# Kernel tuning notes

Measured on AMD Instinct MI355X. Metric: run time of the kernel, lower is better.

The kernel has to match this reference:

```python
import jax, jax.numpy as jnp
import numpy as np

EPS = 1e-5

def _layer_norm(x, gamma, beta):
    mu = jnp.mean(x, axis=-1, keepdims=True)
    var = jnp.mean(jnp.square(x - mu), axis=-1, keepdims=True)
    return (x - mu) * jax.lax.rsqrt(var + EPS) * gamma + beta

def setup_inputs() -> dict:
    key = jax.random.key(0)
    ks = jax.random.split(key, 6)
    B, D, H = 8192, 1024, 1024
    x = jax.random.normal(ks[0], (B, D), dtype=jnp.float32)
    h0 = jax.random.normal(ks[1], (B, H), dtype=jnp.float32)
    c0 = jax.random.normal(ks[2], (B, H), dtype=jnp.float32)
    # learned params (orthogonal init approximated by scaled normal for reference purposes)
    weight_h = jax.random.normal(ks[3], (H, 4 * H), dtype=jnp.float32) / np.sqrt(H)
    weight_x = jax.random.normal(ks[4], (D, 4 * H), dtype=jnp.float32) / np.sqrt(D)
    bias = jnp.zeros((4 * H,), dtype=jnp.float32).at[:H].set(1.0)  # forget-gate bias init to 1
    ln1_g = jnp.ones((4 * H,), jnp.float32); ln1_b = jnp.zeros((4 * H,), jnp.float32)
    ln2_g = jnp.ones((4 * H,), jnp.float32); ln2_b = jnp.zeros((4 * H,), jnp.float32)
    ln3_g = jnp.ones((H,), jnp.float32); ln3_b = jnp.zeros((H,), jnp.float32)
    return {"x": x, "h0": h0, "c0": c0, "weight_h": weight_h, "weight_x": weight_x,
            "bias": bias, "ln1_g": ln1_g, "ln1_b": ln1_b, "ln2_g": ln2_g, "ln2_b": ln2_b,
            "ln3_g": ln3_g, "ln3_b": ln3_b}

def reference(x, h0, c0, weight_h, weight_x, bias, ln1_g, ln1_b, ln2_g, ln2_b, ln3_g, ln3_b):
    # gates: [B, 4H] = LN(h0 @ Wh) + LN(x @ Wx) + bias
    gates = _layer_norm(h0 @ weight_h, ln1_g, ln1_b) + _layer_norm(x @ weight_x, ln2_g, ln2_b) + bias
    H = h0.shape[-1]
    f_g, i_g, o_g, c_g = jnp.split(gates, 4, axis=1)  # forget, in, out, cell
    c1 = jax.nn.sigmoid(f_g) * c0 + jax.nn.sigmoid(i_g) * jnp.tanh(c_g)
    h1 = jax.nn.sigmoid(o_g) * jnp.tanh(_layer_norm(c1, ln3_g, ln3_b))
    return (h1, c1)
```

## Files before the change

kernel.cpp:

```cpp
#include <hip/hip_runtime.h>
#include <cstdint>

#define B_ROWS 8192
#define KDIM 1024
#define N4 4096

typedef __attribute__((ext_vector_type(8))) short short8;
typedef __attribute__((ext_vector_type(4))) float float4v;

__device__ __forceinline__ unsigned short f2bf(float f) {
  union { float f; unsigned int u; } v; v.f = f;
  unsigned int r = v.u + 0x7fffu + ((v.u >> 16) & 1u);
  return (unsigned short)(r >> 16);
}

__device__ __forceinline__ float bf2f(unsigned short s) {
  union { unsigned int u; float f; } v; v.u = ((unsigned int)s) << 16;
  return v.f;
}

__device__ __forceinline__ void async16(const unsigned short* g, unsigned short* l) {
  auto gp = (const __attribute__((address_space(1))) unsigned int*)(uintptr_t)g;
  auto lp = (__attribute__((address_space(3))) unsigned int*)(unsigned int)(uintptr_t)l;
  __builtin_amdgcn_global_load_lds(gp, lp, 16, 0, 0);
}

__device__ __forceinline__ float sigm(float v) {
  return __builtin_amdgcn_rcpf(1.f + __builtin_amdgcn_exp2f(-1.44269504088896f * v));
}
__device__ __forceinline__ float tanh_f(float v) {
  return 1.f - 2.f * __builtin_amdgcn_rcpf(1.f + __builtin_amdgcn_exp2f(2.88539008177793f * v));
}


__global__ __launch_bounds__(256) void prep(
    const float* __restrict__ h0, const float* __restrict__ x,
    unsigned short* __restrict__ Ah, unsigned short* __restrict__ Ax,
    const float* __restrict__ Wh, const float* __restrict__ Wx,
    unsigned short* __restrict__ Wth, unsigned short* __restrict__ Wtx) {
  __shared__ float tile[32][33];
  const int bid = blockIdx.x;
  if (bid < 16384) {
    const float* in = (bid >= 8192) ? x : h0;
    unsigned short* out = (bid >= 8192) ? Ax : Ah;
    int i = ((bid & 8191) * 256 + threadIdx.x) * 4;
    float4 v = *(const float4*)(in + i);
    ushort4 o;
    o.x = f2bf(v.x); o.y = f2bf(v.y); o.z = f2bf(v.z); o.w = f2bf(v.w);
    *(ushort4*)(out + i) = o;
  } else {
    int b2 = bid - 16384;
    const float* W = (b2 >= 4096) ? Wx : Wh;
    unsigned short* Wt = (b2 >= 4096) ? Wtx : Wth;
    int r = b2 & 4095;
    int n0 = (r & 127) * 32;
    int k0 = (r >> 7) * 32;
    int tx = threadIdx.x & 31;
    int ty = threadIdx.x >> 5;
#pragma unroll
    for (int i = 0; i < 32; i += 8)
      tile[ty + i][tx] = W[(size_t)(k0 + ty + i) * N4 + n0 + tx];
    __syncthreads();
#pragma unroll
    for (int i = 0; i < 32; i += 8)
      Wt[(size_t)(n0 + ty + i) * KDIM + k0 + tx] = f2bf(tile[tx][ty + i]);
  }
}


#define LGKM0()  asm volatile("s_waitcnt lgkmcnt(0)" ::: "memory")
#define SCHED0() __builtin_amdgcn_sched_barrier(0)
#define BARRIER() __builtin_amdgcn_s_barrier()
#define VM4BAR() asm volatile("s_waitcnt vmcnt(4)\n\ts_barrier" ::: "memory")

__global__ __launch_bounds__(512, 2) void gemm_bf16(
    const unsigned short* __restrict__ Ah, const unsigned short* __restrict__ Wth,
    unsigned short* __restrict__ Uh,
    const unsigned short* __restrict__ Ax, const unsigned short* __restrict__ Wtx,
    unsigned short* __restrict__ Ux, int row0) {
  const unsigned short* A; const unsigned short* W; unsigned short* U;
  if (blockIdx.z == 0) { A = Ah; W = Wth; U = Uh; } else { A = Ax; W = Wtx; U = Ux; }

  __shared__ unsigned short ldsA[2 * 256 * 64];
  __shared__ unsigned short ldsB[2 * 256 * 64];

  const int tid = threadIdx.x;
  const int wave = tid >> 6;
  const int lane = tid & 63;
  const int wm2 = wave >> 2;
  const int wn4 = wave & 3;

  const int gx = N4 / 256;
  const int nwg = gx * (int)gridDim.y;
  const int f = (int)blockIdx.y * gx + (int)blockIdx.x;
  const int qq = nwg >> 3, rr = nwg & 7;
  const int xcd = f & 7, idx = f >> 3;
  const int wg = (xcd < rr) ? (xcd * (qq + 1) + idx)
                            : (rr * (qq + 1) + (xcd - rr) * qq + idx);
  const int bx = wg & (gx - 1);
  const int by = wg / gx;

  const int m0 = row0 + by * 256;
  const int n0 = bx * 256;

  const int r8 = lane >> 3;
  const int c8 = lane & 7;
  const int g8 = ((c8 - r8) & 7) * 8;
  const int aR = wave * 32;
  const int bR = wave * 32;

  const unsigned short* gA = A + (size_t)(m0 + aR + r8) * KDIM + g8;
  const unsigned short* gB = W + (size_t)(n0 + bR + r8) * KDIM + g8;

  const int lq = lane & 15, lh = lane >> 4;
  const int offA0 = (wm2 * 128 + lq) * 64 + ((lh + lq) & 7) * 8;
  const int offA1 = (wm2 * 128 + lq) * 64 + ((4 + lh + lq) & 7) * 8;
  const int offB0 = (wn4 * 64 + lq) * 64 + ((lh + lq) & 7) * 8;
  const int offB1 = (wn4 * 64 + lq) * 64 + ((4 + lh + lq) & 7) * 8;

  float4v acc[8][4];
  float4v zero = {0.f, 0.f, 0.f, 0.f};
#pragma unroll
  for (int i = 0; i < 8; ++i)
#pragma unroll
    for (int j = 0; j < 4; ++j) acc[i][j] = zero;

#define STAGE4(gp, lb, kk)                                        \
  do {                                                            \
    async16((gp) + (kk), (lb));                                   \
    async16((gp) + (kk) + 8 * KDIM, (lb) + 8 * 64);               \
    async16((gp) + (kk) + 16 * KDIM, (lb) + 16 * 64);             \
    async16((gp) + (kk) + 24 * KDIM, (lb) + 24 * 64);             \
  } while (0)

  STAGE4(gB, ldsB + bR * 64, 0);
  STAGE4(gA, ldsA + aR * 64, 0);
  STAGE4(gB, ldsB + 16384 + bR * 64, 64);
  VM4BAR();

  short8 aF0[8], aF1[8], bF0[4], bF1[4];

  for (int t = 0; t < KDIM / 64; ++t) {
    const unsigned short* sA = ldsA + (t & 1) * 16384;
    const unsigned short* sB = ldsB + (t & 1) * 16384;
    unsigned short* nA = (unsigned short*)ldsA + ((t + 1) & 1) * 16384;
    unsigned short* cB = (unsigned short*)ldsB + (t & 1) * 16384;
    const int kA = (t + 1) * 64;
    const int kB = (t + 2) * 64;

    STAGE4(gA, nA + aR * 64, kA);

#pragma unroll
    for (int mi = 0; mi < 8; ++mi) aF0[mi] = *(const short8*)(sA + offA0 + mi * 1024);
#pragma unroll
    for (int nj = 0; nj < 4; ++nj) bF0[nj] = *(const short8*)(sB + offB0 + nj * 1024);
#pragma unroll
    for (int mi = 0; mi < 8; ++mi) aF1[mi] = *(const short8*)(sA + offA1 + mi * 1024);
#pragma unroll
    for (int nj = 0; nj < 4; ++nj) bF1[nj] = *(const short8*)(sB + offB1 + nj * 1024);

    __builtin_amdgcn_s_setprio(1);
#pragma unroll
    for (int mi = 0; mi < 8; ++mi)
#pragma unroll
      for (int nj = 0; nj < 4; ++nj)
        acc[mi][nj] = __builtin_amdgcn_mfma_f32_16x16x32_bf16(aF0[mi], bF0[nj], acc[mi][nj], 0, 0, 0);
    __builtin_amdgcn_s_setprio(0);

    LGKM0(); SCHED0();
    BARRIER();

    STAGE4(gB, cB + bR * 64, kB);

    __builtin_amdgcn_s_setprio(1);
#pragma unroll
    for (int mi = 0; mi < 8; ++mi)
#pragma unroll
      for (int nj = 0; nj < 4; ++nj)
        acc[mi][nj] = __builtin_amdgcn_mfma_f32_16x16x32_bf16(aF1[mi], bF1[nj], acc[mi][nj], 0, 0, 0);
    __builtin_amdgcn_s_setprio(0);

    VM4BAR();
  }
  asm volatile("s_waitcnt vmcnt(0)" ::: "memory");

  const int colc = lane & 15;
  const int rowq = (lane >> 4) * 4;
  unsigned short* Ub = U + (size_t)(by * 256 + wm2 * 128 + rowq) * N4 + n0 + wn4 * 64 + colc;
#pragma unroll
  for (int mi = 0; mi < 8; ++mi)
#pragma unroll
    for (int r = 0; r < 4; ++r) {
      unsigned short* Urow = Ub + (size_t)(mi * 16 + r) * N4;
#pragma unroll
      for (int nj = 0; nj < 4; ++nj) Urow[nj * 16] = f2bf(acc[mi][nj][r]);
    }
}


__global__ __launch_bounds__(256) void fused_ln_lstm(
    const unsigned short* __restrict__ Uh, const unsigned short* __restrict__ Ux,
    const float* __restrict__ c0, const float* __restrict__ bias,
    const float* __restrict__ g1, const float* __restrict__ b1,
    const float* __restrict__ g2, const float* __restrict__ b2,
    const float* __restrict__ g3, const float* __restrict__ b3,
    float* __restrict__ h1o, float* __restrict__ c1o, int row0) {
  const int t = threadIdx.x;
  const int lane = t & 63;
  const int wv = t >> 6;
  const size_t rloc = blockIdx.x;
  const size_t rabs = rloc + (size_t)row0;

  const ushort4* uh = (const ushort4*)(Uh + rloc * N4);
  const ushort4* ux = (const ushort4*)(Ux + rloc * N4);
  float4 cold = ((const float4*)(c0 + rabs * KDIM))[t];

  float4 vh[4], vx[4];
  float sh = 0.f, qh = 0.f, sx = 0.f, qx = 0.f;
#pragma unroll
  for (int k = 0; k < 4; ++k) {
    ushort4 au = uh[k * 256 + t];
    float4 a; a.x = bf2f(au.x); a.y = bf2f(au.y); a.z = bf2f(au.z); a.w = bf2f(au.w);
    vh[k] = a;
    sh += (a.x + a.y) + (a.z + a.w);
    qh += a.x * a.x + a.y * a.y + a.z * a.z + a.w * a.w;
    ushort4 bu = ux[k * 256 + t];
    float4 b; b.x = bf2f(bu.x); b.y = bf2f(bu.y); b.z = bf2f(bu.z); b.w = bf2f(bu.w);
    vx[k] = b;
    sx += (b.x + b.y) + (b.z + b.w);
    qx += b.x * b.x + b.y * b.y + b.z * b.z + b.w * b.w;
  }
  __shared__ float red[4][4];
#pragma unroll
  for (int o = 32; o > 0; o >>= 1) {
    sh += __shfl_down(sh, o); qh += __shfl_down(qh, o);
    sx += __shfl_down(sx, o); qx += __shfl_down(qx, o);
  }
  if (lane == 0) { red[wv][0] = sh; red[wv][1] = qh; red[wv][2] = sx; red[wv][3] = qx; }
  __syncthreads();
  sh = red[0][0] + red[1][0] + red[2][0] + red[3][0];
  qh = red[0][1] + red[1][1] + red[2][1] + red[3][1];
  sx = red[0][2] + red[1][2] + red[2][2] + red[3][2];
  qx = red[0][3] + red[1][3] + red[2][3] + red[3][3];
  const float inv4 = 1.f / 4096.f;
  const float muh = sh * inv4, mux = sx * inv4;
  const float rsh = rsqrtf(qh * inv4 - muh * muh + 1e-5f);
  const float rsx = rsqrtf(qx * inv4 - mux * mux + 1e-5f);

  float4 gate[4];
#pragma unroll
  for (int k = 0; k < 4; ++k) {
    int j = k * 256 + t;
    float4 G1 = ((const float4*)g1)[j], B1 = ((const float4*)b1)[j];
    float4 G2 = ((const float4*)g2)[j], B2 = ((const float4*)b2)[j];
    float4 BB = ((const float4*)bias)[j];
    float4 a = vh[k], b = vx[k], r;
    r.x = (a.x - muh) * rsh * G1.x + B1.x + (b.x - mux) * rsx * G2.x + B2.x + BB.x;
    r.y = (a.y - muh) * rsh * G1.y + B1.y + (b.y - mux) * rsx * G2.y + B2.y + BB.y;
    r.z = (a.z - muh) * rsh * G1.z + B1.z + (b.z - mux) * rsx * G2.z + B2.z + BB.z;
    r.w = (a.w - muh) * rsh * G1.w + B1.w + (b.w - mux) * rsx * G2.w + B2.w + BB.w;
    gate[k] = r;
  }
  float4 fg = gate[0], ig = gate[1], og = gate[2], cg = gate[3];
  float4 c1v;
  c1v.x = sigm(fg.x) * cold.x + sigm(ig.x) * tanh_f(cg.x);
  c1v.y = sigm(fg.y) * cold.y + sigm(ig.y) * tanh_f(cg.y);
  c1v.z = sigm(fg.z) * cold.z + sigm(ig.z) * tanh_f(cg.z);
  c1v.w = sigm(fg.w) * cold.w + sigm(ig.w) * tanh_f(cg.w);

  float sc = (c1v.x + c1v.y) + (c1v.z + c1v.w);
  float qc = c1v.x * c1v.x + c1v.y * c1v.y + c1v.z * c1v.z + c1v.w * c1v.w;
#pragma unroll
  for (int o = 32; o > 0; o >>= 1) { sc += __shfl_down(sc, o); qc += __shfl_down(qc, o); }
  __syncthreads();
  if (lane == 0) { red[wv][0] = sc; red[wv][1] = qc; }
  __syncthreads();
  sc = red[0][0] + red[1][0] + red[2][0] + red[3][0];
  qc = red[0][1] + red[1][1] + red[2][1] + red[3][1];
  const float invH = 1.f / 1024.f;
  const float muc = sc * invH;
  const float rsc = rsqrtf(qc * invH - muc * muc + 1e-5f);
  float4 G3 = ((const float4*)g3)[t], B3 = ((const float4*)b3)[t];
  float4 h1v;
  h1v.x = sigm(og.x) * tanh_f((c1v.x - muc) * rsc * G3.x + B3.x);
  h1v.y = sigm(og.y) * tanh_f((c1v.y - muc) * rsc * G3.y + B3.y);
  h1v.z = sigm(og.z) * tanh_f((c1v.z - muc) * rsc * G3.z + B3.z);
  h1v.w = sigm(og.w) * tanh_f((c1v.w - muc) * rsc * G3.w + B3.w);

  ((float4*)(h1o + rabs * KDIM))[t] = h1v;
  ((float4*)(c1o + rabs * KDIM))[t] = c1v;
}


extern "C" void kernel_launch(void* const* d_in, const int* in_sizes, int n_in,
                              void* d_out, int out_size, void* d_ws, size_t ws_size,
                              hipStream_t stream) {
  const float* x    = (const float*)d_in[0];
  const float* h0   = (const float*)d_in[1];
  const float* c0   = (const float*)d_in[2];
  const float* Wh   = (const float*)d_in[3];
  const float* Wx   = (const float*)d_in[4];
  const float* bias = (const float*)d_in[5];
  const float* g1   = (const float*)d_in[6];
  const float* b1   = (const float*)d_in[7];
  const float* g2   = (const float*)d_in[8];
  const float* b2   = (const float*)d_in[9];
  const float* g3   = (const float*)d_in[10];
  const float* b3   = (const float*)d_in[11];
  float* h1o = (float*)d_out;
  float* c1o = h1o + (size_t)B_ROWS * KDIM;

  unsigned short* Ah  = (unsigned short*)d_ws;
  unsigned short* Ax  = Ah + (size_t)B_ROWS * KDIM;
  unsigned short* Wth = Ax + (size_t)B_ROWS * KDIM;
  unsigned short* Wtx = Wth + (size_t)N4 * KDIM;
  unsigned short* U = Wtx + (size_t)N4 * KDIM;
  size_t used = ((size_t)B_ROWS * KDIM * 2 + (size_t)N4 * KDIM * 2) * sizeof(unsigned short);
  size_t rem = ws_size > used ? ws_size - used : 0;
  int chunk = (int)(rem / ((size_t)2 * N4 * sizeof(unsigned short)));
  chunk &= ~255;
  if (chunk > B_ROWS) chunk = B_ROWS;
  if (chunk < 256) chunk = 256;

  prep<<<24576, 256, 0, stream>>>(h0, x, Ah, Ax, Wh, Wx, Wth, Wtx);

  for (int r0 = 0; r0 < B_ROWS; r0 += chunk) {
    int rows = chunk;
    if (r0 + rows > B_ROWS) rows = B_ROWS - r0;
    unsigned short* Uh = U;
    unsigned short* Ux = U + (size_t)rows * N4;
    gemm_bf16<<<dim3(N4 / 256, rows / 256, 2), 512, 0, stream>>>(Ah, Wth, Uh, Ax, Wtx, Ux, r0);
    fused_ln_lstm<<<rows, 256, 0, stream>>>(Uh, Ux, c0, bias, g1, b1, g2, b2, g3, b3, h1o, c1o, r0);
  }
}
```

Before: 368.8 us.

## Use 4 waves with 128x128 per-wave tiles in bf16 GEMM

```diff
diff --git a/kernel.cpp b/kernel.cpp
--- a/kernel.cpp
+++ b/kernel.cpp
@@ -71,9 +71,14 @@
 #define LGKM0()  asm volatile("s_waitcnt lgkmcnt(0)" ::: "memory")
 #define SCHED0() __builtin_amdgcn_sched_barrier(0)
 #define BARRIER() __builtin_amdgcn_s_barrier()
-#define VM4BAR() asm volatile("s_waitcnt vmcnt(4)\n\ts_barrier" ::: "memory")
-
-__global__ __launch_bounds__(512, 2) void gemm_bf16(
+
+__device__ __forceinline__ void stage8(const unsigned short* gp, unsigned short* lb, int kk) {
+#pragma unroll
+  for (int j = 0; j < 8; ++j)
+    async16(gp + kk + j * 8 * KDIM, lb + j * 8 * 64);
+}
+
+__global__ __launch_bounds__(256, 1) void gemm_bf16(
     const unsigned short* __restrict__ Ah, const unsigned short* __restrict__ Wth,
     unsigned short* __restrict__ Uh,
     const unsigned short* __restrict__ Ax, const unsigned short* __restrict__ Wtx,
@@ -87,8 +92,8 @@
   const int tid = threadIdx.x;
   const int wave = tid >> 6;
   const int lane = tid & 63;
-  const int wm2 = wave >> 2;
-  const int wn4 = wave & 3;
+  const int wm = (wave & 1) * 128;
+  const int wn = (wave >> 1) * 128;
 
   const int gx = N4 / 256;
   const int nwg = gx * (int)gridDim.y;
@@ -106,39 +111,31 @@
   const int r8 = lane >> 3;
   const int c8 = lane & 7;
   const int g8 = ((c8 - r8) & 7) * 8;
-  const int aR = wave * 32;
-  const int bR = wave * 32;
+  const int aR = wave * 64;
+  const int bR = wave * 64;
 
   const unsigned short* gA = A + (size_t)(m0 + aR + r8) * KDIM + g8;
   const unsigned short* gB = W + (size_t)(n0 + bR + r8) * KDIM + g8;
 
   const int lq = lane & 15, lh = lane >> 4;
-  const int offA0 = (wm2 * 128 + lq) * 64 + ((lh + lq) & 7) * 8;
-  const int offA1 = (wm2 * 128 + lq) * 64 + ((4 + lh + lq) & 7) * 8;
-  const int offB0 = (wn4 * 64 + lq) * 64 + ((lh + lq) & 7) * 8;
-  const int offB1 = (wn4 * 64 + lq) * 64 + ((4 + lh + lq) & 7) * 8;
-
-  float4v acc[8][4];
+  const int offA0 = (wm + lq) * 64 + ((lh + lq) & 7) * 8;
+  const int offA1 = (wm + lq) * 64 + ((4 + lh + lq) & 7) * 8;
+  const int offB0 = (wn + lq) * 64 + ((lh + lq) & 7) * 8;
+  const int offB1 = (wn + lq) * 64 + ((4 + lh + lq) & 7) * 8;
+
+  float4v acc[8][8];
   float4v zero = {0.f, 0.f, 0.f, 0.f};
 #pragma unroll
   for (int i = 0; i < 8; ++i)
 #pragma unroll
-    for (int j = 0; j < 4; ++j) acc[i][j] = zero;
-
-#define STAGE4(gp, lb, kk)                                        \
-  do {                                                            \
-    async16((gp) + (kk), (lb));                                   \
-    async16((gp) + (kk) + 8 * KDIM, (lb) + 8 * 64);               \
-    async16((gp) + (kk) + 16 * KDIM, (lb) + 16 * 64);             \
-    async16((gp) + (kk) + 24 * KDIM, (lb) + 24 * 64);             \
-  } while (0)
-
-  STAGE4(gB, ldsB + bR * 64, 0);
-  STAGE4(gA, ldsA + aR * 64, 0);
-  STAGE4(gB, ldsB + 16384 + bR * 64, 64);
-  VM4BAR();
-
-  short8 aF0[8], aF1[8], bF0[4], bF1[4];
+    for (int j = 0; j < 8; ++j) acc[i][j] = zero;
+
+  stage8(gB, ldsB + bR * 64, 0);
+  stage8(gA, ldsA + aR * 64, 0);
+  stage8(gB, ldsB + 16384 + bR * 64, 64);
+  asm volatile("s_waitcnt vmcnt(8)\n\ts_barrier" ::: "memory");
+
+  short8 aF[8], bFa[8], bFb[8];
 
   for (int t = 0; t < KDIM / 64; ++t) {
     const unsigned short* sA = ldsA + (t & 1) * 16384;
@@ -148,52 +145,53 @@
     const int kA = (t + 1) * 64;
     const int kB = (t + 2) * 64;
 
-    STAGE4(gA, nA + aR * 64, kA);
-
-#pragma unroll
-    for (int mi = 0; mi < 8; ++mi) aF0[mi] = *(const short8*)(sA + offA0 + mi * 1024);
-#pragma unroll
-    for (int nj = 0; nj < 4; ++nj) bF0[nj] = *(const short8*)(sB + offB0 + nj * 1024);
-#pragma unroll
-    for (int mi = 0; mi < 8; ++mi) aF1[mi] = *(const short8*)(sA + offA1 + mi * 1024);
-#pragma unroll
-    for (int nj = 0; nj < 4; ++nj) bF1[nj] = *(const short8*)(sB + offB1 + nj * 1024);
+    stage8(gA, nA + aR * 64, kA);
+
+#pragma unroll
+    for (int i = 0; i < 8; ++i) aF[i]  = *(const short8*)(sA + offA0 + i * 1024);
+#pragma unroll
+    for (int j = 0; j < 8; ++j) bFa[j] = *(const short8*)(sB + offB0 + j * 1024);
+#pragma unroll
+    for (int j = 0; j < 8; ++j) bFb[j] = *(const short8*)(sB + offB1 + j * 1024);
 
     __builtin_amdgcn_s_setprio(1);
 #pragma unroll
-    for (int mi = 0; mi < 8; ++mi)
-#pragma unroll
-      for (int nj = 0; nj < 4; ++nj)
-        acc[mi][nj] = __builtin_amdgcn_mfma_f32_16x16x32_bf16(aF0[mi], bF0[nj], acc[mi][nj], 0, 0, 0);
+    for (int i = 0; i < 8; ++i)
+#pragma unroll
+      for (int j = 0; j < 8; ++j)
+        acc[i][j] = __builtin_amdgcn_mfma_f32_16x16x32_bf16(aF[i], bFa[j], acc[i][j], 0, 0, 0);
     __builtin_amdgcn_s_setprio(0);
 
     LGKM0(); SCHED0();
     BARRIER();
 
-    STAGE4(gB, cB + bR * 64, kB);
+    stage8(gB, cB + bR * 64, kB);
+
+#pragma unroll
+    for (int i = 0; i < 8; ++i) aF[i] = *(const short8*)(sA + offA1 + i * 1024);
 
     __builtin_amdgcn_s_setprio(1);
 #pragma unroll
-    for (int mi = 0; mi < 8; ++mi)
-#pragma unroll
-      for (int nj = 0; nj < 4; ++nj)
-        acc[mi][nj] = __builtin_amdgcn_mfma_f32_16x16x32_bf16(aF1[mi], bF1[nj], acc[mi][nj], 0, 0, 0);
+    for (int i = 0; i < 8; ++i)
+#pragma unroll
+      for (int j = 0; j < 8; ++j)
+        acc[i][j] = __builtin_amdgcn_mfma_f32_16x16x32_bf16(aF[i], bFb[j], acc[i][j], 0, 0, 0);
     __builtin_amdgcn_s_setprio(0);
 
-    VM4BAR();
+    asm volatile("s_waitcnt vmcnt(8)\n\ts_barrier" ::: "memory");
   }
   asm volatile("s_waitcnt vmcnt(0)" ::: "memory");
 
   const int colc = lane & 15;
   const int rowq = (lane >> 4) * 4;
-  unsigned short* Ub = U + (size_t)(by * 256 + wm2 * 128 + rowq) * N4 + n0 + wn4 * 64 + colc;
+  unsigned short* Ub = U + (size_t)(by * 256 + wm + rowq) * N4 + n0 + wn + colc;
 #pragma unroll
   for (int mi = 0; mi < 8; ++mi)
 #pragma unroll
     for (int r = 0; r < 4; ++r) {
       unsigned short* Urow = Ub + (size_t)(mi * 16 + r) * N4;
 #pragma unroll
-      for (int nj = 0; nj < 4; ++nj) Urow[nj * 16] = f2bf(acc[mi][nj][r]);
+      for (int nj = 0; nj < 8; ++nj) Urow[nj * 16] = f2bf(acc[mi][nj][r]);
     }
 }
 
@@ -329,7 +327,7 @@
     if (r0 + rows > B_ROWS) rows = B_ROWS - r0;
     unsigned short* Uh = U;
     unsigned short* Ux = U + (size_t)rows * N4;
-    gemm_bf16<<<dim3(N4 / 256, rows / 256, 2), 512, 0, stream>>>(Ah, Wth, Uh, Ax, Wtx, Ux, r0);
+    gemm_bf16<<<dim3(N4 / 256, rows / 256, 2), 256, 0, stream>>>(Ah, Wth, Uh, Ax, Wtx, Ux, r0);
     fused_ln_lstm<<<rows, 256, 0, stream>>>(Uh, Ux, c0, bias, g1, b1, g2, b2, g3, b3, h1o, c1o, r0);
   }
 }
```

Measured after the change: 378.1 us. 1.03x slower.
